# Kernel optimization log

Hardware: AMD Instinct MI355X
Metric: run time of the kernel (lower is better)

## Reference

```python
import jax, jax.numpy as jnp
import numpy as np

N = 100000
E = 1600000
F_IN = 256
H1, C1 = 8, 8          # conv1: 8 heads x 8 channels -> 64
H2, C2 = 1, 32         # conv2: 1 head x num_classes
SLOPE = 0.2


def gat_conv(x, src, dst, n, W, a_src, a_dst, b, heads, out):
    # x: [n, f_in]; W: [f_in, heads*out]; a_src/a_dst: [heads, out]; b: [heads*out]
    h = (x @ W).reshape(n, heads, out)                       # [n, H, C]
    s = jnp.sum(h * a_src, axis=-1)                          # [n, H]
    d = jnp.sum(h * a_dst, axis=-1)                          # [n, H]
    e = jax.nn.leaky_relu(s[src] + d[dst], SLOPE)            # [e, H]
    m = jax.ops.segment_max(e, dst, num_segments=n)          # stable segment softmax
    ex = jnp.exp(e - m[dst])
    z = jax.ops.segment_sum(ex, dst, num_segments=n)
    alpha = ex / (z[dst] + 1e-16)                            # [e, H]
    msg = alpha[:, :, None] * h[src]                         # [e, H, C]
    agg = jax.ops.segment_sum(msg, dst, num_segments=n)      # [n, H, C]
    return agg.reshape(n, heads * out) + b


def setup_inputs() -> dict:
    key = jax.random.key(0)
    ks = jax.random.split(key, 10)
    x = jax.random.normal(ks[0], (N, F_IN), dtype=jnp.float32)
    edge_index = jax.random.randint(ks[1], (2, E), 0, N, dtype=jnp.int32)
    sc = 0.05
    W1 = jax.random.normal(ks[2], (F_IN, H1 * C1), dtype=jnp.float32) * sc
    att_src1 = jax.random.normal(ks[3], (H1, C1), dtype=jnp.float32) * sc
    att_dst1 = jax.random.normal(ks[4], (H1, C1), dtype=jnp.float32) * sc
    b1 = jnp.zeros((H1 * C1,), dtype=jnp.float32)
    W2 = jax.random.normal(ks[5], (H1 * C1, H2 * C2), dtype=jnp.float32) * sc
    att_src2 = jax.random.normal(ks[6], (H2, C2), dtype=jnp.float32) * sc
    att_dst2 = jax.random.normal(ks[7], (H2, C2), dtype=jnp.float32) * sc
    b2 = jnp.zeros((H2 * C2,), dtype=jnp.float32)
    return {"x": x, "edge_index": edge_index, "W1": W1, "att_src1": att_src1,
            "att_dst1": att_dst1, "b1": b1, "W2": W2, "att_src2": att_src2,
            "att_dst2": att_dst2, "b2": b2}


def reference(x, edge_index, W1, att_src1, att_dst1, b1, W2, att_src2, att_dst2, b2):
    # add self loops (PyG GATConv default)
    loops = jnp.arange(N, dtype=edge_index.dtype)
    src = jnp.concatenate([edge_index[0], loops])
    dst = jnp.concatenate([edge_index[1], loops])
    # dropout layers are identity in eval mode
    h = gat_conv(x, src, dst, N, W1, att_src1, att_dst1, b1, H1, C1)
    h = jax.nn.elu(h)
    h = gat_conv(h, src, dst, N, W2, att_src2, att_dst2, b2, H2, C2)
    return jax.nn.log_softmax(h, axis=1)
```

## Files before the change

### kernel.cpp

```cpp
#include <hip/hip_runtime.h>
#include <hip/hip_bf16.h>

#define N_NODES 100000
#define N_EDGES 1600000
#define N_TOT   (N_EDGES + N_NODES)
#define F_IN    256
#define F1      64
#define H1      8
#define C1      8
#define F2      32
#define SLOPE   0.2f

#define NB_G2   ((N_NODES + 63) / 64)

#define EB      4096
#define NB1     ((N_EDGES + EB - 1) / EB)
#define BW      256
#define NBKT    ((N_NODES + BW - 1) / BW)

typedef unsigned int  uint;
typedef unsigned short ushort;
typedef __attribute__((ext_vector_type(8))) short bf16x8;
typedef __attribute__((ext_vector_type(4))) float f32x4;
typedef __attribute__((ext_vector_type(2))) float f32x2;

__device__ inline ushort f2bf(float f) {
    uint u = __float_as_uint(f);
    uint r = u + 0x7fffu + ((u >> 16) & 1u);
    return (ushort)(r >> 16);
}
__device__ inline float bflo(uint u) { return __uint_as_float(u << 16); }
__device__ inline float bfhi(uint u) { return __uint_as_float(u & 0xffff0000u); }
__device__ inline uint pk2bf(float a, float b) {
    __hip_bfloat162 h = __float22bfloat162_rn(make_float2(a, b));
    union { __hip_bfloat162 h; uint u; } cv; cv.h = h;
    return cv.u;
}

__device__ inline void bucket_bases(const int* __restrict__ colsum,
                                    int* sc, int* sb, int tid) {
    const int i0 = 2 * tid, i1 = 2 * tid + 1;
    const int a0 = (i0 < NBKT) ? colsum[i0] : 0;
    const int a1 = (i1 < NBKT) ? colsum[i1] : 0;
    sc[tid] = a0 + a1;
    __syncthreads();
    for (int off = 1; off < 256; off <<= 1) {
        int t = (tid >= off) ? sc[tid - off] : 0;
        __syncthreads();
        sc[tid] += t;
        __syncthreads();
    }
    const int excl = sc[tid] - (a0 + a1);
    if (i0 < NBKT)  sb[i0] = excl;
    if (i1 <= NBKT) sb[i1] = excl + a0;
    __syncthreads();
}

__global__ __launch_bounds__(256) void k_p1w(
        const int* __restrict__ ei, const float* __restrict__ W1,
        int* __restrict__ bcnt, ushort* __restrict__ w1b) {
    __shared__ int H[NBKT];
    const int tid = threadIdx.x;
    if (blockIdx.x == NB1) {
        for (int i = 0; i < 64; ++i) {
            const int e = i * 256 + tid;
            const int k = e >> 6, n = e & 63;
            w1b[((k >> 3) * 64 + n) * 8 + (k & 7)] = f2bf(W1[e]);
        }
        return;
    }
    const int blk = blockIdx.x;
    for (int j = tid; j < NBKT; j += 256) H[j] = 0;
    __syncthreads();
    const int e0 = blk * EB;
    const int lim = (e0 + EB < N_EDGES) ? e0 + EB : N_EDGES;
    for (int i = e0 + tid * 2; i < lim; i += 512) {
        const int2 dd = *(const int2*)&ei[N_EDGES + i];
        atomicAdd(&H[dd.x >> 8], 1);
        atomicAdd(&H[dd.y >> 8], 1);
    }
    __syncthreads();
    for (int j = tid; j < NBKT; j += 256)
        bcnt[j * NB1 + blk] = H[j];
}

__global__ __launch_bounds__(64) void k_p2(
        int* __restrict__ bcnt, int* __restrict__ colsum) {
    const int col = blockIdx.x, lane = threadIdx.x;
    int carry = 0;
    for (int c0 = 0; c0 < NB1; c0 += 64) {
        const int idx = c0 + lane;
        const int v = (idx < NB1) ? bcnt[col * NB1 + idx] : 0;
        int s = v;
#pragma unroll
        for (int off = 1; off < 64; off <<= 1) {
            int u = __shfl_up(s, off);
            if (lane >= off) s += u;
        }
        if (idx < NB1) bcnt[col * NB1 + idx] = carry + s - v;
        carry += __shfl(s, 63);
    }
    if (lane == 0) colsum[col] = carry;
}

__global__ __launch_bounds__(256) void k_p3(
        const int* __restrict__ ei, const int* __restrict__ bcnt,
        const int* __restrict__ colsum, uint* __restrict__ tmp) {
    __shared__ int sc[256];
    __shared__ int cur[NBKT + 1];
    const int tid = threadIdx.x, blk = blockIdx.x;
    bucket_bases(colsum, sc, cur, tid);
    for (int b = tid; b < NBKT; b += 256) cur[b] += bcnt[b * NB1 + blk];
    __syncthreads();
    const int e0 = blk * EB;
    const int lim = (e0 + EB < N_EDGES) ? e0 + EB : N_EDGES;
    for (int i = e0 + tid * 2; i < lim; i += 512) {
        const int2 ss = *(const int2*)&ei[i];
        const int2 dd = *(const int2*)&ei[N_EDGES + i];
        const int p0 = atomicAdd(&cur[dd.x >> 8], 1);
        tmp[p0] = ((uint)(dd.x & 255) << 24) | (uint)ss.x;
        const int p1 = atomicAdd(&cur[dd.y >> 8], 1);
        tmp[p1] = ((uint)(dd.y & 255) << 24) | (uint)ss.y;
    }
}

__global__ __launch_bounds__(256) void k_final_gemm(
        const uint* __restrict__ tmp, const int* __restrict__ colsum,
        int* __restrict__ row_ptr, int* __restrict__ srcs,
        const float* __restrict__ x, const ushort* __restrict__ w1b,
        const float* __restrict__ as1, const float* __restrict__ ad1,
        ushort* __restrict__ h1b, float* __restrict__ s1,
        float* __restrict__ d1) {
    __shared__ union {
        struct { int sc[256]; int sb[NBKT + 1]; int cur[BW]; } f;
        ushort S[4][16][66];
    } sm;
    const int tid = threadIdx.x;

    if (blockIdx.x < NBKT) {
        const int b = blockIdx.x;
        bucket_bases(colsum, sm.f.sc, sm.f.sb, tid);
        sm.f.cur[tid] = 0;
        __syncthreads();
        const int lo = sm.f.sb[b], hi = sm.f.sb[b + 1];
        for (int i = lo + tid; i < hi; i += 256)
            atomicAdd(&sm.f.cur[tmp[i] >> 24], 1);
        __syncthreads();
        const int n = b * BW + tid;
        const int myc = sm.f.cur[tid];
        const int v = (n < N_NODES) ? myc + 1 : 0;
        __syncthreads();
        sm.f.sc[tid] = v;
        __syncthreads();
        for (int off = 1; off < 256; off <<= 1) {
            int t = (tid >= off) ? sm.f.sc[tid - off] : 0;
            __syncthreads();
            sm.f.sc[tid] += t;
            __syncthreads();
        }
        const int rp = lo + b * BW + (sm.f.sc[tid] - v);
        if (n < N_NODES) {
            row_ptr[n] = rp;
            srcs[rp] = n;
        }
        if (b == NBKT - 1 && tid == 255) row_ptr[N_NODES] = N_TOT;
        sm.f.cur[tid] = rp + 1;
        __syncthreads();
        for (int i = lo + tid; i < hi; i += 256) {
            const uint u = tmp[i];
            const int pos = atomicAdd(&sm.f.cur[u >> 24], 1);
            srcs[pos] = (int)(u & 0xFFFFFFu);
        }
        return;
    }

    const int wave = tid >> 6, lane = tid & 63;
    const int q = lane >> 4, ln = lane & 15;
    const int rowbase = (blockIdx.x - NBKT) * 64 + wave * 16;
    const int row = rowbase + ln;
    const int rowc = row < N_NODES ? row : N_NODES - 1;
    const float* xr = x + (size_t)rowc * F_IN + q * 8;

    f32x4 acc[4];
#pragma unroll
    for (int nt = 0; nt < 4; ++nt) acc[nt] = (f32x4){0.f, 0.f, 0.f, 0.f};

#pragma unroll 4
    for (int t = 0; t < 8; ++t) {
        const float4 a0 = *(const float4*)(xr + t * 32);
        const float4 a1 = *(const float4*)(xr + t * 32 + 4);
        uint4 au = make_uint4(pk2bf(a0.x, a0.y), pk2bf(a0.z, a0.w),
                              pk2bf(a1.x, a1.y), pk2bf(a1.z, a1.w));
        bf16x8 af = *(bf16x8*)&au;
        bf16x8 bfr[4];
#pragma unroll
        for (int nt = 0; nt < 4; ++nt)
            bfr[nt] = *(const bf16x8*)&w1b[((t * 4 + q) * 64 + nt * 16 + ln) * 8];
#pragma unroll
        for (int nt = 0; nt < 4; ++nt)
            acc[nt] = __builtin_amdgcn_mfma_f32_16x16x32_bf16(
                          af, bfr[nt], acc[nt], 0, 0, 0);
    }

#pragma unroll
    for (int nt = 0; nt < 4; ++nt)
#pragma unroll
        for (int r = 0; r < 4; ++r)
            sm.S[wave][q * 4 + r][nt * 16 + ln] = f2bf(acc[nt][r]);
    __builtin_amdgcn_wave_barrier();

    if (lane >= 16) return;
    const int node = rowbase + lane;
    if (node >= N_NODES) return;
    const uint* srow = (const uint*)&sm.S[wave][lane][0];
    float sacc[H1], dacc[H1];
#pragma unroll
    for (int h = 0; h < H1; ++h) { sacc[h] = 0.f; dacc[h] = 0.f; }
    uint4* hout = (uint4*)(h1b + (size_t)node * F1);
#pragma unroll
    for (int p4 = 0; p4 < 8; ++p4) {
        const uint u0 = srow[p4 * 4 + 0], u1 = srow[p4 * 4 + 1];
        const uint u2 = srow[p4 * 4 + 2], u3 = srow[p4 * 4 + 3];
        hout[p4] = make_uint4(u0, u1, u2, u3);
        const float c[8] = {bflo(u0), bfhi(u0), bflo(u1), bfhi(u1),
                            bflo(u2), bfhi(u2), bflo(u3), bfhi(u3)};
#pragma unroll
        for (int j = 0; j < 8; ++j) {
            sacc[p4] += c[j] * as1[p4 * 8 + j];
            dacc[p4] += c[j] * ad1[p4 * 8 + j];
        }
    }
    float4* s4 = (float4*)(s1 + (size_t)node * H1);
    float4* d4 = (float4*)(d1 + (size_t)node * H1);
    s4[0] = make_float4(sacc[0], sacc[1], sacc[2], sacc[3]);
    s4[1] = make_float4(sacc[4], sacc[5], sacc[6], sacc[7]);
    d4[0] = make_float4(dacc[0], dacc[1], dacc[2], dacc[3]);
    d4[1] = make_float4(dacc[4], dacc[5], dacc[6], dacc[7]);
}

__global__ __launch_bounds__(256) void k_agg1(
        const int* __restrict__ row_ptr, const int* __restrict__ srcs,
        const ushort* __restrict__ h1b, const float* __restrict__ s1,
        const float* __restrict__ d1, const float* __restrict__ b1,
        const float* __restrict__ W2, const float* __restrict__ as2,
        const float* __restrict__ ad2,
        ushort* __restrict__ h2b, float* __restrict__ s2,
        float* __restrict__ d2) {
    __shared__ float sx[4][64];
    const int wid = (blockIdx.x * 256 + threadIdx.x) >> 6;
    if (wid >= N_NODES) return;
    const int w = threadIdx.x >> 6;
    const int lane = threadIdx.x & 63;
    const int q = lane >> 2;
    const int cp = lane & 3;
    const float2 dh2 = *(const float2*)((const char*)d1 + (size_t)wid * 32 + 8 * cp);
    const int beg = row_ptr[wid], end = row_ptr[wid + 1];
    const char* hP = (const char*)h1b;
    const char* sP = (const char*)s1;
    const uint hOff = 32u * (uint)cp;
    const uint sOff = 8u * (uint)cp;
    f32x2 A0 = {0.f, 0.f}, A1 = {0.f, 0.f}, A2 = {0.f, 0.f}, A3 = {0.f, 0.f};
    f32x2 A4 = {0.f, 0.f}, A5 = {0.f, 0.f}, A6 = {0.f, 0.f}, A7 = {0.f, 0.f};
    f32x2 z2 = {0.f, 0.f};
    for (int i = beg + q; i < end; i += 16) {
        const int nA = srcs[i];
        const float2 sv2 = *(const float2*)(sP + ((uint)nA * 32u + sOff));
        float e0 = sv2.x + dh2.x, e1 = sv2.y + dh2.y;
        e0 = fmaxf(e0, SLOPE * e0);
        e1 = fmaxf(e1, SLOPE * e1);
        const float x0 = __expf(e0), x1 = __expf(e1);
        const uint base = (uint)nA * 128u + hOff;
        const uint4 U0 = *(const uint4*)(hP + base);
        const uint4 U1 = *(const uint4*)(hP + base + 16);
        z2 += (f32x2){x0, x1};
        const f32x2 xa0 = {x0, x0}, xa1 = {x1, x1};
        A0 += xa0 * (f32x2){bflo(U0.x), bfhi(U0.x)};
        A1 += xa0 * (f32x2){bflo(U0.y), bfhi(U0.y)};
        A2 += xa0 * (f32x2){bflo(U0.z), bfhi(U0.z)};
        A3 += xa0 * (f32x2){bflo(U0.w), bfhi(U0.w)};
        A4 += xa1 * (f32x2){bflo(U1.x), bfhi(U1.x)};
        A5 += xa1 * (f32x2){bflo(U1.y), bfhi(U1.y)};
        A6 += xa1 * (f32x2){bflo(U1.z), bfhi(U1.z)};
        A7 += xa1 * (f32x2){bflo(U1.w), bfhi(U1.w)};
    }
    f32x2 r0, r1, r2, r3;
    float zf;
    {
        const bool hi = lane & 4;
        f32x2 s0 = hi ? A0 : A4, s1v = hi ? A1 : A5;
        f32x2 s2v = hi ? A2 : A6, s3v = hi ? A3 : A7;
        const f32x2 k0 = hi ? A4 : A0, k1 = hi ? A5 : A1;
        const f32x2 k2 = hi ? A6 : A2, k3 = hi ? A7 : A3;
        s0.x = __shfl_xor(s0.x, 4); s0.y = __shfl_xor(s0.y, 4);
        s1v.x = __shfl_xor(s1v.x, 4); s1v.y = __shfl_xor(s1v.y, 4);
        s2v.x = __shfl_xor(s2v.x, 4); s2v.y = __shfl_xor(s2v.y, 4);
        s3v.x = __shfl_xor(s3v.x, 4); s3v.y = __shfl_xor(s3v.y, 4);
        r0 = k0 + s0; r1 = k1 + s1v; r2 = k2 + s2v; r3 = k3 + s3v;
        float zs = hi ? z2.x : z2.y;
        const float zk = hi ? z2.y : z2.x;
        zs = __shfl_xor(zs, 4);
        zf = zk + zs;
    }
    {
        const bool hi = lane & 8;
        f32x2 s0 = hi ? r0 : r2, s1v = hi ? r1 : r3;
        const f32x2 k0 = hi ? r2 : r0, k1 = hi ? r3 : r1;
        s0.x = __shfl_xor(s0.x, 8); s0.y = __shfl_xor(s0.y, 8);
        s1v.x = __shfl_xor(s1v.x, 8); s1v.y = __shfl_xor(s1v.y, 8);
        r0 = k0 + s0; r1 = k1 + s1v;
    }
    {
        const bool hi = lane & 16;
        f32x2 s0 = hi ? r0 : r1;
        const f32x2 k0 = hi ? r1 : r0;
        s0.x = __shfl_xor(s0.x, 16); s0.y = __shfl_xor(s0.y, 16);
        r0 = k0 + s0;
    }
    float sv;
    {
        const bool hi = lane & 32;
        float s0 = hi ? r0.x : r0.y;
        const float k0 = hi ? r0.y : r0.x;
        s0 = __shfl_xor(s0, 32);
        sv = k0 + s0;
    }
    zf += __shfl_xor(zf, 8); zf += __shfl_xor(zf, 16); zf += __shfl_xor(zf, 32);

    const int xi = cp * 16 + ((lane >> 2) & 1) * 8 + ((lane >> 3) & 1) * 4
                 + ((lane >> 4) & 1) * 2 + ((lane >> 5) & 1);
    const float zi = 1.f / (zf + 1e-16f);
    float xv = sv * zi + b1[xi];
    xv = xv > 0.f ? xv : __expf(xv) - 1.f;
    sx[w][xi] = xv;
    __builtin_amdgcn_wave_barrier();

    const int kh = lane >> 5;
    const int oc = lane & 31;
    const float4* sxv = (const float4*)&sx[w][kh * 32];
    const float* wp0 = W2 + (size_t)(kh * 32) * F2 + oc;
    float acc = 0.f;
#pragma unroll
    for (int k4 = 0; k4 < 8; ++k4) {
        const float4 xv4 = sxv[k4];
        const float* wp = wp0 + (size_t)k4 * 4 * F2;
        acc += xv4.x * wp[0]      + xv4.y * wp[F2]
             + xv4.z * wp[2 * F2] + xv4.w * wp[3 * F2];
    }
    acc += __shfl_xor(acc, 32);

    float sA2 = acc * as2[oc], dA2 = acc * ad2[oc];
#pragma unroll
    for (int off = 1; off <= 16; off <<= 1) {
        sA2 += __shfl_xor(sA2, off);
        dA2 += __shfl_xor(dA2, off);
    }
    const float accp = __shfl_xor(acc, 1);
    if (lane < 32 && !(lane & 1))
        *(uint*)&h2b[(size_t)wid * F2 + oc] = pk2bf(acc, accp);
    if (lane == 0) { s2[wid] = sA2; d2[wid] = dA2; }
}

__global__ __launch_bounds__(256) void k_agg2(
        const int* __restrict__ row_ptr, const int* __restrict__ srcs,
        const ushort* __restrict__ h2b, const float* __restrict__ s2,
        const float* __restrict__ d2, const float* __restrict__ b2,
        float* __restrict__ out) {
    const int wid = (blockIdx.x * 256 + threadIdx.x) >> 6;
    if (wid >= N_NODES) return;
    const int lane = threadIdx.x & 63;
    const int q = lane >> 1;
    const int ch = lane & 1;
    const float dn = d2[wid];
    const int beg = row_ptr[wid], end = row_ptr[wid + 1];
    const char* hP = (const char*)h2b;
    const char* sP = (const char*)s2;
    const uint ch32 = 32u * (uint)ch;
    f32x2 A0 = {0.f, 0.f}, A1 = {0.f, 0.f}, A2 = {0.f, 0.f}, A3 = {0.f, 0.f};
    f32x2 A4 = {0.f, 0.f}, A5 = {0.f, 0.f}, A6 = {0.f, 0.f}, A7 = {0.f, 0.f};
    float z = 0.f;
    for (int i = beg + q; i < end; i += 32) {
        const int nA = srcs[i];
        float eA = *(const float*)(sP + (uint)nA * 4u) + dn;
        eA = fmaxf(eA, SLOPE * eA);
        const float xA = __expf(eA);
        const uint off = (uint)nA * 64u + ch32;
        const uint4 U0 = *(const uint4*)(hP + off);
        const uint4 U1 = *(const uint4*)(hP + off + 16);
        z += xA;
        const f32x2 xa = {xA, xA};
        A0 += xa * (f32x2){bflo(U0.x), bfhi(U0.x)};
        A1 += xa * (f32x2){bflo(U0.y), bfhi(U0.y)};
        A2 += xa * (f32x2){bflo(U0.z), bfhi(U0.z)};
        A3 += xa * (f32x2){bflo(U0.w), bfhi(U0.w)};
        A4 += xa * (f32x2){bflo(U1.x), bfhi(U1.x)};
        A5 += xa * (f32x2){bflo(U1.y), bfhi(U1.y)};
        A6 += xa * (f32x2){bflo(U1.z), bfhi(U1.z)};
        A7 += xa * (f32x2){bflo(U1.w), bfhi(U1.w)};
    }
    f32x2 r0, r1, r2, r3;
    {
        const bool hi = lane & 2;
        f32x2 s0 = hi ? A0 : A4, s1v = hi ? A1 : A5;
        f32x2 s2v = hi ? A2 : A6, s3v = hi ? A3 : A7;
        const f32x2 k0 = hi ? A4 : A0, k1 = hi ? A5 : A1;
        const f32x2 k2 = hi ? A6 : A2, k3 = hi ? A7 : A3;
        s0.x = __shfl_xor(s0.x, 2); s0.y = __shfl_xor(s0.y, 2);
        s1v.x = __shfl_xor(s1v.x, 2); s1v.y = __shfl_xor(s1v.y, 2);
        s2v.x = __shfl_xor(s2v.x, 2); s2v.y = __shfl_xor(s2v.y, 2);
        s3v.x = __shfl_xor(s3v.x, 2); s3v.y = __shfl_xor(s3v.y, 2);
        r0 = k0 + s0; r1 = k1 + s1v; r2 = k2 + s2v; r3 = k3 + s3v;
    }
    {
        const bool hi = lane & 4;
        f32x2 s0 = hi ? r0 : r2, s1v = hi ? r1 : r3;
        const f32x2 k0 = hi ? r2 : r0, k1 = hi ? r3 : r1;
        s0.x = __shfl_xor(s0.x, 4); s0.y = __shfl_xor(s0.y, 4);
        s1v.x = __shfl_xor(s1v.x, 4); s1v.y = __shfl_xor(s1v.y, 4);
        r0 = k0 + s0; r1 = k1 + s1v;
    }
    {
        const bool hi = lane & 8;
        f32x2 s0 = hi ? r0 : r1;
        const f32x2 k0 = hi ? r1 : r0;
        s0.x = __shfl_xor(s0.x, 8); s0.y = __shfl_xor(s0.y, 8);
        r0 = k0 + s0;
    }
    float sv;
    {
        const bool hi = lane & 16;
        float s0 = hi ? r0.x : r0.y;
        const float k0 = hi ? r0.y : r0.x;
        s0 = __shfl_xor(s0, 16);
        sv = k0 + s0;
    }
    sv += __shfl_xor(sv, 32);
    z += __shfl_xor(z, 2); z += __shfl_xor(z, 4); z += __shfl_xor(z, 8);
    z += __shfl_xor(z, 16); z += __shfl_xor(z, 32);

    const int elem = ch * 16 + ((lane >> 1) & 1) * 8 + ((lane >> 2) & 1) * 4
                   + ((lane >> 3) & 1) * 2 + ((lane >> 4) & 1);
    const float zi = 1.f / (z + 1e-16f);
    const float v = sv * zi + b2[elem];
    float m = v;
#pragma unroll
    for (int off = 1; off <= 16; off <<= 1) m = fmaxf(m, __shfl_xor(m, off));
    float ssum = __expf(v - m);
#pragma unroll
    for (int off = 1; off <= 16; off <<= 1) ssum += __shfl_xor(ssum, off);
    const float lse = m + __logf(ssum);
    if (lane < 32) out[(size_t)wid * F2 + elem] = v - lse;
}

extern "C" void kernel_launch(void* const* d_in, const int* in_sizes, int n_in,
                              void* d_out, int out_size, void* d_ws, size_t ws_size,
                              hipStream_t stream) {
    const float* x   = (const float*)d_in[0];
    const int*   ei  = (const int*)d_in[1];
    const float* W1  = (const float*)d_in[2];
    const float* as1 = (const float*)d_in[3];
    const float* ad1 = (const float*)d_in[4];
    const float* b1  = (const float*)d_in[5];
    const float* W2  = (const float*)d_in[6];
    const float* as2 = (const float*)d_in[7];
    const float* ad2 = (const float*)d_in[8];
    const float* b2  = (const float*)d_in[9];
    float* out = (float*)d_out;

    ushort* h1b = (ushort*)d_ws;
    ushort* h2b = h1b + (size_t)N_NODES * F1;
    ushort* w1b = h2b + (size_t)N_NODES * F2;
    float*  s1  = (float*)(w1b + F_IN * F1);
    float*  d1  = s1 + (size_t)N_NODES * H1;
    float*  s2  = d1 + (size_t)N_NODES * H1;
    float*  d2  = s2 + N_NODES;
    uint*   tmp = (uint*)(d2 + N_NODES);
    int* row_ptr = (int*)(tmp + N_EDGES);
    int* colsum  = row_ptr + N_NODES + 1;
    int* bcnt    = colsum + NBKT;
    int* srcs    = bcnt + (size_t)NBKT * NB1;

    const int nb_w = (N_NODES * 64 + 255) / 256;

    k_p1w<<<NB1 + 1, 256, 0, stream>>>(ei, W1, bcnt, w1b);
    k_p2<<<NBKT, 64, 0, stream>>>(bcnt, colsum);
    k_p3<<<NB1, 256, 0, stream>>>(ei, bcnt, colsum, tmp);
    k_final_gemm<<<NBKT + NB_G2, 256, 0, stream>>>(tmp, colsum, row_ptr, srcs,
                                                   x, w1b, as1, ad1,
                                                   h1b, s1, d1);
    k_agg1<<<nb_w, 256, 0, stream>>>(row_ptr, srcs, h1b, s1, d1, b1,
                                     W2, as2, ad2, h2b, s2, d2);
    k_agg2<<<nb_w, 256, 0, stream>>>(row_ptr, srcs, h2b, s2, d2, b2, out);
}
```

Before: 333.8 us.

## Replace three-pass bucket sort with single-pass atomic-reserved fixed-capacity buckets

Merges the histogram, column-scan and scatter kernels into one sort kernel. Each block reserves space in fixed-capacity per-bucket slots (MAXB entries) through global atomics on per-bucket counters, which are zeroed by a memset beforehand. This removes two kernel launches and the global count matrix traffic. In exchange, edge order within a bucket becomes nondeterministic, and a bucket holding more than MAXB edges would overflow into the next bucket's slot, which is safe only for roughly uniform degree distributions.

```diff
diff --git a/kernel.cpp b/kernel.cpp
--- a/kernel.cpp
+++ b/kernel.cpp
@@ -17,6 +17,7 @@
 #define NB1     ((N_EDGES + EB - 1) / EB)
 #define BW      256
 #define NBKT    ((N_NODES + BW - 1) / BW)
+#define MAXB    5120
 
 typedef unsigned int  uint;
 typedef unsigned short ushort;
@@ -37,11 +38,11 @@
     return cv.u;
 }
 
-__device__ inline void bucket_bases(const int* __restrict__ colsum,
+__device__ inline void bucket_bases(const int* __restrict__ cnts,
                                     int* sc, int* sb, int tid) {
     const int i0 = 2 * tid, i1 = 2 * tid + 1;
-    const int a0 = (i0 < NBKT) ? colsum[i0] : 0;
-    const int a1 = (i1 < NBKT) ? colsum[i1] : 0;
+    const int a0 = (i0 < NBKT) ? cnts[i0] : 0;
+    const int a1 = (i1 < NBKT) ? cnts[i1] : 0;
     sc[tid] = a0 + a1;
     __syncthreads();
     for (int off = 1; off < 256; off <<= 1) {
@@ -56,10 +57,11 @@
     __syncthreads();
 }
 
-__global__ __launch_bounds__(256) void k_p1w(
+__global__ __launch_bounds__(256) void k_sort(
         const int* __restrict__ ei, const float* __restrict__ W1,
-        int* __restrict__ bcnt, ushort* __restrict__ w1b) {
-    __shared__ int H[NBKT];
+        int* __restrict__ gcnt, uint* __restrict__ tmp,
+        ushort* __restrict__ w1b) {
+    __shared__ int HC[NBKT];
     const int tid = threadIdx.x;
     if (blockIdx.x == NB1) {
         for (int i = 0; i < 64; ++i) {
@@ -70,62 +72,34 @@
         return;
     }
     const int blk = blockIdx.x;
-    for (int j = tid; j < NBKT; j += 256) H[j] = 0;
+    for (int j = tid; j < NBKT; j += 256) HC[j] = 0;
     __syncthreads();
     const int e0 = blk * EB;
     const int lim = (e0 + EB < N_EDGES) ? e0 + EB : N_EDGES;
     for (int i = e0 + tid * 2; i < lim; i += 512) {
         const int2 dd = *(const int2*)&ei[N_EDGES + i];
-        atomicAdd(&H[dd.x >> 8], 1);
-        atomicAdd(&H[dd.y >> 8], 1);
+        atomicAdd(&HC[dd.x >> 8], 1);
+        atomicAdd(&HC[dd.y >> 8], 1);
     }
     __syncthreads();
-    for (int j = tid; j < NBKT; j += 256)
-        bcnt[j * NB1 + blk] = H[j];
-}
-
-__global__ __launch_bounds__(64) void k_p2(
-        int* __restrict__ bcnt, int* __restrict__ colsum) {
-    const int col = blockIdx.x, lane = threadIdx.x;
-    int carry = 0;
-    for (int c0 = 0; c0 < NB1; c0 += 64) {
-        const int idx = c0 + lane;
-        const int v = (idx < NB1) ? bcnt[col * NB1 + idx] : 0;
-        int s = v;
-#pragma unroll
-        for (int off = 1; off < 64; off <<= 1) {
-            int u = __shfl_up(s, off);
-            if (lane >= off) s += u;
-        }
-        if (idx < NB1) bcnt[col * NB1 + idx] = carry + s - v;
-        carry += __shfl(s, 63);
-    }
-    if (lane == 0) colsum[col] = carry;
-}
-
-__global__ __launch_bounds__(256) void k_p3(
-        const int* __restrict__ ei, const int* __restrict__ bcnt,
-        const int* __restrict__ colsum, uint* __restrict__ tmp) {
-    __shared__ int sc[256];
-    __shared__ int cur[NBKT + 1];
-    const int tid = threadIdx.x, blk = blockIdx.x;
-    bucket_bases(colsum, sc, cur, tid);
-    for (int b = tid; b < NBKT; b += 256) cur[b] += bcnt[b * NB1 + blk];
+    for (int b = tid; b < NBKT; b += 256) {
+        const int c = HC[b];
+        const int base = c ? atomicAdd(&gcnt[b], c) : 0;
+        HC[b] = b * MAXB + base;
+    }
     __syncthreads();
-    const int e0 = blk * EB;
-    const int lim = (e0 + EB < N_EDGES) ? e0 + EB : N_EDGES;
     for (int i = e0 + tid * 2; i < lim; i += 512) {
         const int2 ss = *(const int2*)&ei[i];
         const int2 dd = *(const int2*)&ei[N_EDGES + i];
-        const int p0 = atomicAdd(&cur[dd.x >> 8], 1);
+        const int p0 = atomicAdd(&HC[dd.x >> 8], 1);
         tmp[p0] = ((uint)(dd.x & 255) << 24) | (uint)ss.x;
-        const int p1 = atomicAdd(&cur[dd.y >> 8], 1);
+        const int p1 = atomicAdd(&HC[dd.y >> 8], 1);
         tmp[p1] = ((uint)(dd.y & 255) << 24) | (uint)ss.y;
     }
 }
 
 __global__ __launch_bounds__(256) void k_final_gemm(
-        const uint* __restrict__ tmp, const int* __restrict__ colsum,
+        const uint* __restrict__ tmp, const int* __restrict__ gcnt,
         int* __restrict__ row_ptr, int* __restrict__ srcs,
         const float* __restrict__ x, const ushort* __restrict__ w1b,
         const float* __restrict__ as1, const float* __restrict__ ad1,
@@ -139,10 +113,11 @@
 
     if (blockIdx.x < NBKT) {
         const int b = blockIdx.x;
-        bucket_bases(colsum, sm.f.sc, sm.f.sb, tid);
+        bucket_bases(gcnt, sm.f.sc, sm.f.sb, tid);
         sm.f.cur[tid] = 0;
         __syncthreads();
-        const int lo = sm.f.sb[b], hi = sm.f.sb[b + 1];
+        const int lo = b * MAXB;
+        const int hi = lo + (sm.f.sb[b + 1] - sm.f.sb[b]);
         for (int i = lo + tid; i < hi; i += 256)
             atomicAdd(&sm.f.cur[tmp[i] >> 24], 1);
         __syncthreads();
@@ -158,7 +133,7 @@
             sm.f.sc[tid] += t;
             __syncthreads();
         }
-        const int rp = lo + b * BW + (sm.f.sc[tid] - v);
+        const int rp = sm.f.sb[b] + b * BW + (sm.f.sc[tid] - v);
         if (n < N_NODES) {
             row_ptr[n] = rp;
             srcs[rp] = n;
@@ -473,18 +448,16 @@
     float*  d1  = s1 + (size_t)N_NODES * H1;
     float*  s2  = d1 + (size_t)N_NODES * H1;
     float*  d2  = s2 + N_NODES;
-    uint*   tmp = (uint*)(d2 + N_NODES);
-    int* row_ptr = (int*)(tmp + N_EDGES);
-    int* colsum  = row_ptr + N_NODES + 1;
-    int* bcnt    = colsum + NBKT;
-    int* srcs    = bcnt + (size_t)NBKT * NB1;
+    int*    gcnt = (int*)(d2 + N_NODES);
+    uint*   tmp = (uint*)(gcnt + NBKT);
+    int* row_ptr = (int*)(tmp + (size_t)NBKT * MAXB);
+    int* srcs    = row_ptr + N_NODES + 1;
 
     const int nb_w = (N_NODES * 64 + 255) / 256;
 
-    k_p1w<<<NB1 + 1, 256, 0, stream>>>(ei, W1, bcnt, w1b);
-    k_p2<<<NBKT, 64, 0, stream>>>(bcnt, colsum);
-    k_p3<<<NB1, 256, 0, stream>>>(ei, bcnt, colsum, tmp);
-    k_final_gemm<<<NBKT + NB_G2, 256, 0, stream>>>(tmp, colsum, row_ptr, srcs,
+    hipMemsetAsync(gcnt, 0, (size_t)NBKT * sizeof(int), stream);
+    k_sort<<<NB1 + 1, 256, 0, stream>>>(ei, W1, gcnt, tmp, w1b);
+    k_final_gemm<<<NBKT + NB_G2, 256, 0, stream>>>(tmp, gcnt, row_ptr, srcs,
                                                    x, w1b, as1, ad1,
                                                    h1b, s1, d1);
     k_agg1<<<nb_w, 256, 0, stream>>>(row_ptr, srcs, h1b, s1, d1, b1,
```

After: 326.0 us. -2.4%, faster.
